# Performance work log

Hardware: AMD Instinct MI355X
Metric: run time of the kernel (lower is better)

Reference implementation:

```python
import jax, jax.numpy as jnp
import numpy as np

B, L, S, H = 2, 256, 384, 768
Tc, Dc = 16, 50
WV, WD = 20000, 100
CV = 128
NEG = -1e30


def _lstm_scan(x, Wih, Whh, bih, bhh):
    # x: [N, T, D] -> hs: [N, T, Hc]; torch LSTM gate order i,f,g,o
    N = x.shape[0]
    Hc = Whh.shape[1]
    h0 = jnp.zeros((N, Hc), x.dtype)

    def step(carry, xt):
        h, c = carry
        g = xt @ Wih.T + h @ Whh.T + bih + bhh  # [N, 4Hc]
        i, f, gg, o = jnp.split(g, 4, axis=-1)
        i = jax.nn.sigmoid(i)
        f = jax.nn.sigmoid(f)
        gg = jnp.tanh(gg)
        o = jax.nn.sigmoid(o)
        c = f * c + i * gg
        h = o * jnp.tanh(c)
        return (h, c), h

    _, hs = jax.lax.scan(step, (h0, h0), jnp.swapaxes(x, 0, 1))
    return jnp.swapaxes(hs, 0, 1)


def setup_inputs() -> dict:
    key = jax.random.key(0)
    ks = jax.random.split(key, 10)
    bert_emb = jax.random.normal(ks[0], (B, S, H), jnp.float32)
    pieces2word = jax.random.randint(ks[1], (B, L, S), 0, 2, jnp.int32)
    word_ids = jax.random.randint(ks[2], (B, L), 0, WV, jnp.int32)
    char_count = jax.random.randint(ks[3], (B, L), 1, Tc + 1, jnp.int32)
    char_ids = jax.random.randint(ks[4], (B, L, Tc), 0, CV, jnp.int32)
    # mask consistent with ragged char lengths (first char_count positions valid)
    token_masks_char = (jnp.arange(Tc)[None, None, :] < char_count[..., None]).astype(jnp.int32)
    word_table = jax.random.normal(ks[5], (WV, WD), jnp.float32) * 0.02
    char_table = jax.random.normal(ks[6], (CV, Dc), jnp.float32) * 0.02
    sc = 1.0 / np.sqrt(Dc)

    def lstm_w(k):
        a, b, c, d = jax.random.split(k, 4)
        return (jax.random.uniform(a, (4 * Dc, Dc), jnp.float32, -sc, sc),
                jax.random.uniform(b, (4 * Dc, Dc), jnp.float32, -sc, sc),
                jax.random.uniform(c, (4 * Dc,), jnp.float32, -sc, sc),
                jax.random.uniform(d, (4 * Dc,), jnp.float32, -sc, sc))

    Wih_f, Whh_f, bih_f, bhh_f = lstm_w(ks[7])
    Wih_b, Whh_b, bih_b, bhh_b = lstm_w(ks[8])
    return dict(bert_emb=bert_emb, pieces2word=pieces2word, word_ids=word_ids,
                char_count=char_count, char_ids=char_ids, token_masks_char=token_masks_char,
                word_table=word_table, char_table=char_table,
                Wih_f=Wih_f, Whh_f=Whh_f, bih_f=bih_f, bhh_f=bhh_f,
                Wih_b=Wih_b, Whh_b=Whh_b, bih_b=bih_b, bhh_b=bhh_b)


def reference(bert_emb, pieces2word, word_ids, char_count, char_ids, token_masks_char,
              word_table, char_table, Wih_f, Whh_f, bih_f, bhh_f, Wih_b, Whh_b, bih_b, bhh_b):
    # --- piece2word max pool (expand + masked_fill(min) + max over pieces) ---
    minv = jnp.min(bert_emb)
    # [B, L, S, H] intermediate, as in the original expand
    masked = jnp.where(pieces2word[..., None] != 0, bert_emb[:, None, :, :], minv)
    word_reps = jnp.max(masked, axis=2)  # [B, L, H]
    # dropouts are identity in eval mode

    # --- word embedding lookup ---
    word_embed = word_table[word_ids]  # [B, L, WD]

    # --- char bi-LSTM with packed-sequence semantics ---
    lens = jnp.maximum(char_count.reshape(-1), 1)  # char_count[char_count==0]=1
    x = char_table[char_ids.reshape(B * L, Tc)]  # [N, Tc, Dc]
    h_fwd = _lstm_scan(x, Wih_f, Whh_f, bih_f, bhh_f)
    # reverse each sequence within its valid length for the backward direction
    t = jnp.arange(Tc)[None, :]
    idx = jnp.where(t < lens[:, None], lens[:, None] - 1 - t, t)  # [N, Tc]
    x_rev = jnp.take_along_axis(x, idx[..., None], axis=1)
    h_bwd = _lstm_scan(x_rev, Wih_b, Whh_b, bih_b, bhh_b)
    h_bwd = jnp.take_along_axis(h_bwd, idx[..., None], axis=1)  # back to original order
    h = jnp.concatenate([h_fwd, h_bwd], axis=-1)  # [N, Tc, 2*Dc]
    valid = (t < lens[:, None])[..., None]
    h = jnp.where(valid, h, 0.0)  # pad_packed_sequence zero-pads beyond length
    h = h.reshape(B, L, Tc, 2 * Dc)

    # --- combine(..., 'max'): masked max over ragged char groups ---
    m = jnp.where(token_masks_char[..., None] == 0, NEG, 0.0)
    sup = jnp.max(m + h, axis=2)  # [B, L, 2*Dc]
    sup = jnp.where(sup == NEG, 0.0, sup)

    return jnp.concatenate([word_reps, word_embed, sup], axis=-1)  # [B, L, H+WD+2*Dc]
```

## Files before the change

kernel.cpp:

```cpp
#include <hip/hip_runtime.h>
#include <float.h>

#define Bb 2
#define Ll 256
#define Ss 384
#define Hh 768
#define Tc 16
#define Dc 50
#define WD 100
#define CV 128
#define NG 200
#define OUTC 968


__device__ inline float tanh_fast(float x) {
    float e = __expf(2.f * x);
    return 1.f - 2.f / (e + 1.f);
}
__device__ inline float sigmoid_fast(float x) {
    return 1.f / (1.f + __expf(-x));
}


__global__ __launch_bounds__(256) void kernel1(
        const float* __restrict__ bert, const float* __restrict__ char_table,
        const float* __restrict__ Wih_f, const float* __restrict__ bih_f, const float* __restrict__ bhh_f,
        const float* __restrict__ Wih_b, const float* __restrict__ bih_b, const float* __restrict__ bhh_b,
        const int* __restrict__ word_ids, const float* __restrict__ word_table,
        float* __restrict__ minp, float* __restrict__ xpt, float* __restrict__ out) {
    int blk = blockIdx.x, tid = threadIdx.x;
    if (blk < 128) {
        const int n4 = (Bb * Ss * Hh) / 4;
        const float4* b4 = (const float4*)bert;
        float m = FLT_MAX;
        for (int i = blk * 256 + tid; i < n4; i += 128 * 256) {
            float4 v = b4[i];
            m = fminf(m, fminf(fminf(v.x, v.y), fminf(v.z, v.w)));
        }
        #pragma unroll
        for (int off = 32; off; off >>= 1) m = fminf(m, __shfl_down(m, off, 64));
        __shared__ float red[4];
        if ((tid & 63) == 0) red[tid >> 6] = m;
        __syncthreads();
        if (tid == 0) minp[blk] = fminf(fminf(red[0], red[1]), fminf(red[2], red[3]));
    } else if (blk < 144) {
        int idx = blk - 128;
        int dir = idx >> 3, c0 = (idx & 7) * 16;
        const float* Wih = dir ? Wih_b : Wih_f;
        const float* bih = dir ? bih_b : bih_f;
        const float* bhh = dir ? bhh_b : bhh_f;
        __shared__ float ct[16][Dc];
        for (int e = tid; e < 16 * Dc; e += 256)
            ((float*)ct)[e] = char_table[c0 * Dc + e];
        __syncthreads();
        if (tid < NG) {
            float w[Dc];
            #pragma unroll
            for (int j = 0; j < Dc; j++) w[j] = Wih[tid * Dc + j];
            float bias = bih[tid] + bhh[tid];
            for (int cid = 0; cid < 16; cid++) {
                float a = bias;
                #pragma unroll
                for (int j = 0; j < Dc; j++) a += w[j] * ct[cid][j];
                xpt[(dir * CV + c0 + cid) * NG + tid] = a;
            }
        }
    } else {
        for (int i = (blk - 144) * 256 + tid; i < Bb * Ll * WD; i += 64 * 256) {
            int bl = i / WD, d = i - bl * WD;
            out[(size_t)bl * OUTC + Hh + d] = word_table[(size_t)word_ids[bl] * WD + d];
        }
    }
}


__global__ __launch_bounds__(256) void kernel2(
        const int* __restrict__ char_ids, const int* __restrict__ char_count,
        const float* __restrict__ Whh_f, const float* __restrict__ Whh_b,
        const float* __restrict__ xpt,
        const float* __restrict__ bert, const int* __restrict__ p2w,
        const float* __restrict__ minp, float* __restrict__ out) {
    __shared__ __align__(16) char smem[13888];
    int blk = blockIdx.x, tid = threadIdx.x;

    if (blk < 1024) {
        float (*xg)[NG] = (float (*)[NG])smem;
        float* gs  = (float*)(smem + 12800);
        float* hs  = (float*)(smem + 13600);
        int*   scid = (int*)(smem + 13808);

        int n = blk >> 1, dir = blk & 1;
        const float* Whh = dir ? Whh_b : Whh_f;

        int len = char_count[n];
        if (len < 1) len = 1;
        if (tid < Tc) {
            int t = tid;
            int st = dir ? (t < len ? len - 1 - t : t) : t;
            scid[t] = char_ids[n * Tc + st];
        }
        if (tid < 52) hs[tid] = 0.f;
        __syncthreads();

        for (int e = tid; e < Tc * (NG / 4); e += 256) {
            int t = e / 50, q = e - t * 50;
            ((float4*)xg[t])[q] = ((const float4*)&xpt[(dir * CV + scid[t]) * NG])[q];
        }
        float w[52];
        if (tid < NG) {
            #pragma unroll
            for (int j = 0; j < Dc; j++) w[j] = Whh[tid * Dc + j];
            w[50] = 0.f; w[51] = 0.f;
        }
        __syncthreads();

        float c = 0.f, maxv = -FLT_MAX;
        for (int t = 0; t < Tc; t++) {
            if (tid < NG) {
                float g = xg[t][tid];
                #pragma unroll
                for (int j = 0; j < 52; j += 4) {
                    float4 hv = *(const float4*)&hs[j];
                    g += hv.x * w[j] + hv.y * w[j+1] + hv.z * w[j+2] + hv.w * w[j+3];
                }
                gs[tid] = g;
            }
            __syncthreads();
            if (tid < Dc) {
                float si = sigmoid_fast(gs[tid]);
                float sf = sigmoid_fast(gs[tid + 50]);
                float tg = tanh_fast(gs[tid + 100]);
                float so = sigmoid_fast(gs[tid + 150]);
                c = sf * c + si * tg;
                float h = so * tanh_fast(c);
                hs[tid] = h;
                if (t < len) maxv = fmaxf(maxv, h);
            }
            __syncthreads();
        }
        if (tid < Dc)
            out[(size_t)n * OUTC + (Hh + WD) + dir * Dc + tid] = maxv;
    } else {
        float (*sacc)[4][128] = (float (*)[4][128])smem;
        float* sminv = (float*)(smem + 8192);

        if (tid < 64) {
            float m = fminf(minp[tid], minp[tid + 64]);
            #pragma unroll
            for (int off = 32; off; off >>= 1) m = fminf(m, __shfl_down(m, off, 64));
            if (tid == 0) *sminv = m;
        }
        int idx = blk - 1024;
        int hc  = idx % 6;
        int lt  = (idx / 6) & 63;
        int b   = idx / 384;
        int l0  = lt * 4;
        int w    = tid >> 6;
        int lane = tid & 63;
        int s0 = w * 96;

        const int* pm = p2w + ((size_t)(b * Ll + l0)) * Ss + s0;
        unsigned m0[4], m1[4], m2[4];
        #pragma unroll
        for (int r = 0; r < 4; r++) {
            unsigned long long b0 = __ballot(pm[r * Ss + lane] != 0);
            unsigned long long b1 = __ballot(lane < 32 ? (pm[r * Ss + 64 + lane] != 0) : false);
            m0[r] = __builtin_amdgcn_readfirstlane((unsigned)b0);
            m1[r] = __builtin_amdgcn_readfirstlane((unsigned)(b0 >> 32));
            m2[r] = __builtin_amdgcn_readfirstlane((unsigned)b1);
        }

        const float2* bb2 = (const float2*)(bert + (size_t)b * Ss * Hh) + hc * 64 + lane;
        float2 acc[4];
        #pragma unroll
        for (int r = 0; r < 4; r++) { acc[r].x = -FLT_MAX; acc[r].y = -FLT_MAX; }

        for (int jo = 0; jo < 96; jo += 8) {
            float2 v[8];
            #pragma unroll
            for (int k = 0; k < 8; k++) v[k] = bb2[(size_t)(s0 + jo + k) * 384];
            #pragma unroll
            for (int k = 0; k < 8; k++) {
                int j = jo + k;
                #pragma unroll
                for (int r = 0; r < 4; r++) {
                    unsigned bit = (j < 32 ? m0[r] >> j
                                 : j < 64 ? m1[r] >> (j - 32)
                                          : m2[r] >> (j - 64)) & 1u;
                    if (bit) {
                        acc[r].x = fmaxf(acc[r].x, v[k].x);
                        acc[r].y = fmaxf(acc[r].y, v[k].y);
                    }
                }
            }
        }
        #pragma unroll
        for (int r = 0; r < 4; r++)
            *(float2*)&sacc[w][r][lane * 2] = acc[r];
        __syncthreads();

        float mv = *sminv;
        #pragma unroll
        for (int e = tid; e < 4 * 128; e += 256) {
            int r = e >> 7, cx = e & 127;
            float m = fmaxf(fmaxf(sacc[0][r][cx], sacc[1][r][cx]),
                            fmaxf(sacc[2][r][cx], sacc[3][r][cx]));
            if (m == -FLT_MAX) m = mv;
            out[((size_t)(b * Ll + l0 + r)) * OUTC + hc * 128 + cx] = m;
        }
    }
}

extern "C" void kernel_launch(void* const* d_in, const int* in_sizes, int n_in,
                              void* d_out, int out_size, void* d_ws, size_t ws_size,
                              hipStream_t stream) {
    const float* bert       = (const float*)d_in[0];
    const int*   p2w        = (const int*)d_in[1];
    const int*   word_ids   = (const int*)d_in[2];
    const int*   char_count = (const int*)d_in[3];
    const int*   char_ids   = (const int*)d_in[4];
    const float* word_table = (const float*)d_in[6];
    const float* char_table = (const float*)d_in[7];
    const float* Wih_f = (const float*)d_in[8];
    const float* Whh_f = (const float*)d_in[9];
    const float* bih_f = (const float*)d_in[10];
    const float* bhh_f = (const float*)d_in[11];
    const float* Wih_b = (const float*)d_in[12];
    const float* Whh_b = (const float*)d_in[13];
    const float* bih_b = (const float*)d_in[14];
    const float* bhh_b = (const float*)d_in[15];
    float* out = (float*)d_out;

    float* minp = (float*)d_ws;
    float* xpt  = minp + 128;

    kernel1<<<208, 256, 0, stream>>>(
        bert, char_table, Wih_f, bih_f, bhh_f, Wih_b, bih_b, bhh_b,
        word_ids, word_table, minp, xpt, out);
    kernel2<<<1792, 256, 0, stream>>>(
        char_ids, char_count, Whh_f, Whh_b, xpt, bert, p2w, minp, out);
}
```

Measured before the change: 124.0 us.

## Rework LSTM recurrence to readlane broadcast, widen pooling tiles, move gather

The char-LSTM block now gives each of four waves one gate (4 waves x 50 lanes), keeps its Whh row and the 16 precomputed input projections in registers, and broadcasts h with readlane. This leaves one barrier per timestep with double-buffered gate storage instead of two barriers and shared-memory h. The bert max-pool blocks now handle 8 words instead of 4, halving block count and re-reads of bert. The word-embedding gather moves from kernel1 into kernel2, and kernel2 gets a launch_bounds occupancy hint; the larger register footprint risks spills or lower occupancy.

```diff
diff --git a/kernel.cpp b/kernel.cpp
--- a/kernel.cpp
+++ b/kernel.cpp
@@ -26,8 +26,7 @@
         const float* __restrict__ bert, const float* __restrict__ char_table,
         const float* __restrict__ Wih_f, const float* __restrict__ bih_f, const float* __restrict__ bhh_f,
         const float* __restrict__ Wih_b, const float* __restrict__ bih_b, const float* __restrict__ bhh_b,
-        const int* __restrict__ word_ids, const float* __restrict__ word_table,
-        float* __restrict__ minp, float* __restrict__ xpt, float* __restrict__ out) {
+        float* __restrict__ minp, float* __restrict__ xpt) {
     int blk = blockIdx.x, tid = threadIdx.x;
     if (blk < 128) {
         const int n4 = (Bb * Ss * Hh) / 4;
@@ -43,7 +42,7 @@
         if ((tid & 63) == 0) red[tid >> 6] = m;
         __syncthreads();
         if (tid == 0) minp[blk] = fminf(fminf(red[0], red[1]), fminf(red[2], red[3]));
-    } else if (blk < 144) {
+    } else {
         int idx = blk - 128;
         int dir = idx >> 3, c0 = (idx & 7) * 16;
         const float* Wih = dir ? Wih_b : Wih_f;
@@ -65,84 +64,72 @@
                 xpt[(dir * CV + c0 + cid) * NG + tid] = a;
             }
         }
-    } else {
-        for (int i = (blk - 144) * 256 + tid; i < Bb * Ll * WD; i += 64 * 256) {
-            int bl = i / WD, d = i - bl * WD;
-            out[(size_t)bl * OUTC + Hh + d] = word_table[(size_t)word_ids[bl] * WD + d];
-        }
     }
 }
 
 
-__global__ __launch_bounds__(256) void kernel2(
+__global__ __launch_bounds__(256, 5) void kernel2(
         const int* __restrict__ char_ids, const int* __restrict__ char_count,
         const float* __restrict__ Whh_f, const float* __restrict__ Whh_b,
         const float* __restrict__ xpt,
         const float* __restrict__ bert, const int* __restrict__ p2w,
-        const float* __restrict__ minp, float* __restrict__ out) {
-    __shared__ __align__(16) char smem[13888];
+        const float* __restrict__ minp,
+        const int* __restrict__ word_ids, const float* __restrict__ word_table,
+        float* __restrict__ out) {
+    __shared__ __align__(16) char smem[16392];
     int blk = blockIdx.x, tid = threadIdx.x;
 
     if (blk < 1024) {
-        float (*xg)[NG] = (float (*)[NG])smem;
-        float* gs  = (float*)(smem + 12800);
-        float* hs  = (float*)(smem + 13600);
-        int*   scid = (int*)(smem + 13808);
-
+        float* gs = (float*)smem;
         int n = blk >> 1, dir = blk & 1;
         const float* Whh = dir ? Whh_b : Whh_f;
+        int w = tid >> 6, l = tid & 63;
+        int lc = l < 50 ? l : 49;
+        int grow = w * 50 + lc;
 
         int len = char_count[n];
         if (len < 1) len = 1;
-        if (tid < Tc) {
-            int t = tid;
+
+        float wr[50];
+        #pragma unroll
+        for (int j = 0; j < 50; j++) wr[j] = Whh[grow * 50 + j];
+
+        float xv[Tc];
+        #pragma unroll
+        for (int t = 0; t < Tc; t++) {
             int st = dir ? (t < len ? len - 1 - t : t) : t;
-            scid[t] = char_ids[n * Tc + st];
-        }
-        if (tid < 52) hs[tid] = 0.f;
-        __syncthreads();
-
-        for (int e = tid; e < Tc * (NG / 4); e += 256) {
-            int t = e / 50, q = e - t * 50;
-            ((float4*)xg[t])[q] = ((const float4*)&xpt[(dir * CV + scid[t]) * NG])[q];
-        }
-        float w[52];
-        if (tid < NG) {
-            #pragma unroll
-            for (int j = 0; j < Dc; j++) w[j] = Whh[tid * Dc + j];
-            w[50] = 0.f; w[51] = 0.f;
-        }
-        __syncthreads();
-
-        float c = 0.f, maxv = -FLT_MAX;
+            int cid = char_ids[n * Tc + st];
+            xv[t] = xpt[(dir * CV + cid) * NG + grow];
+        }
+
+        float c = 0.f, h = 0.f, maxv = -FLT_MAX;
+        #pragma unroll
         for (int t = 0; t < Tc; t++) {
-            if (tid < NG) {
-                float g = xg[t][tid];
-                #pragma unroll
-                for (int j = 0; j < 52; j += 4) {
-                    float4 hv = *(const float4*)&hs[j];
-                    g += hv.x * w[j] + hv.y * w[j+1] + hv.z * w[j+2] + hv.w * w[j+3];
-                }
-                gs[tid] = g;
+            float g0 = xv[t], g1 = 0.f;
+            int hb = __float_as_int(h);
+            #pragma unroll
+            for (int j = 0; j < 50; j += 2) {
+                g0 = fmaf(__int_as_float(__builtin_amdgcn_readlane(hb, j)),     wr[j],     g0);
+                g1 = fmaf(__int_as_float(__builtin_amdgcn_readlane(hb, j + 1)), wr[j + 1], g1);
             }
+            float g = g0 + g1;
+            float act = (w == 2) ? tanh_fast(g) : sigmoid_fast(g);
+            float* gb = gs + (t & 1) * 256;
+            gb[(w << 6) | l] = act;
             __syncthreads();
-            if (tid < Dc) {
-                float si = sigmoid_fast(gs[tid]);
-                float sf = sigmoid_fast(gs[tid + 50]);
-                float tg = tanh_fast(gs[tid + 100]);
-                float so = sigmoid_fast(gs[tid + 150]);
-                c = sf * c + si * tg;
-                float h = so * tanh_fast(c);
-                hs[tid] = h;
-                if (t < len) maxv = fmaxf(maxv, h);
-            }
-            __syncthreads();
-        }
-        if (tid < Dc)
+            float si = gb[lc];
+            float sf = gb[64 + lc];
+            float tg = gb[128 + lc];
+            float so = gb[192 + lc];
+            c = sf * c + si * tg;
+            h = so * tanh_fast(c);
+            if (t < len) maxv = fmaxf(maxv, h);
+        }
+        if (tid < 50)
             out[(size_t)n * OUTC + (Hh + WD) + dir * Dc + tid] = maxv;
-    } else {
-        float (*sacc)[4][128] = (float (*)[4][128])smem;
-        float* sminv = (float*)(smem + 8192);
+    } else if (blk < 1408) {
+        float (*sacc)[8][128] = (float (*)[8][128])smem;
+        float* sminv = (float*)(smem + 16384);
 
         if (tid < 64) {
             float m = fminf(minp[tid], minp[tid + 64]);
@@ -152,17 +139,17 @@
         }
         int idx = blk - 1024;
         int hc  = idx % 6;
-        int lt  = (idx / 6) & 63;
-        int b   = idx / 384;
-        int l0  = lt * 4;
+        int lt  = (idx / 6) & 31;
+        int b   = idx / 192;
+        int l0  = lt * 8;
         int w    = tid >> 6;
         int lane = tid & 63;
         int s0 = w * 96;
 
         const int* pm = p2w + ((size_t)(b * Ll + l0)) * Ss + s0;
-        unsigned m0[4], m1[4], m2[4];
-        #pragma unroll
-        for (int r = 0; r < 4; r++) {
+        unsigned m0[8], m1[8], m2[8];
+        #pragma unroll
+        for (int r = 0; r < 8; r++) {
             unsigned long long b0 = __ballot(pm[r * Ss + lane] != 0);
             unsigned long long b1 = __ballot(lane < 32 ? (pm[r * Ss + 64 + lane] != 0) : false);
             m0[r] = __builtin_amdgcn_readfirstlane((unsigned)b0);
@@ -171,9 +158,9 @@
         }
 
         const float2* bb2 = (const float2*)(bert + (size_t)b * Ss * Hh) + hc * 64 + lane;
-        float2 acc[4];
-        #pragma unroll
-        for (int r = 0; r < 4; r++) { acc[r].x = -FLT_MAX; acc[r].y = -FLT_MAX; }
+        float2 acc[8];
+        #pragma unroll
+        for (int r = 0; r < 8; r++) { acc[r].x = -FLT_MAX; acc[r].y = -FLT_MAX; }
 
         for (int jo = 0; jo < 96; jo += 8) {
             float2 v[8];
@@ -183,7 +170,7 @@
             for (int k = 0; k < 8; k++) {
                 int j = jo + k;
                 #pragma unroll
-                for (int r = 0; r < 4; r++) {
+                for (int r = 0; r < 8; r++) {
                     unsigned bit = (j < 32 ? m0[r] >> j
                                  : j < 64 ? m1[r] >> (j - 32)
                                           : m2[r] >> (j - 64)) & 1u;
@@ -195,18 +182,22 @@
             }
         }
         #pragma unroll
-        for (int r = 0; r < 4; r++)
+        for (int r = 0; r < 8; r++)
             *(float2*)&sacc[w][r][lane * 2] = acc[r];
         __syncthreads();
 
         float mv = *sminv;
-        #pragma unroll
-        for (int e = tid; e < 4 * 128; e += 256) {
+        for (int e = tid; e < 8 * 128; e += 256) {
             int r = e >> 7, cx = e & 127;
             float m = fmaxf(fmaxf(sacc[0][r][cx], sacc[1][r][cx]),
                             fmaxf(sacc[2][r][cx], sacc[3][r][cx]));
             if (m == -FLT_MAX) m = mv;
             out[((size_t)(b * Ll + l0 + r)) * OUTC + hc * 128 + cx] = m;
+        }
+    } else {
+        for (int i = (blk - 1408) * 256 + tid; i < Bb * Ll * WD; i += 64 * 256) {
+            int bl = i / WD, d = i - bl * WD;
+            out[(size_t)bl * OUTC + Hh + d] = word_table[(size_t)word_ids[bl] * WD + d];
         }
     }
 }
@@ -234,9 +225,10 @@
     float* minp = (float*)d_ws;
     float* xpt  = minp + 128;
 
-    kernel1<<<208, 256, 0, stream>>>(
+    kernel1<<<144, 256, 0, stream>>>(
         bert, char_table, Wih_f, bih_f, bhh_f, Wih_b, bih_b, bhh_b,
-        word_ids, word_table, minp, xpt, out);
-    kernel2<<<1792, 256, 0, stream>>>(
-        char_ids, char_count, Whh_f, Whh_b, xpt, bert, p2w, minp, out);
-}
+        minp, xpt);
+    kernel2<<<1472, 256, 0, stream>>>(
+        char_ids, char_count, Whh_f, Whh_b, xpt, bert, p2w, minp,
+        word_ids, word_table, out);
+}
```

Result: slower. 157.2 us (+26.8%).
